# Kernel optimization log

Measured on AMD Instinct MI355X. Metric: run time of the kernel, lower is better.

The kernel has to match this reference:

```python
import jax, jax.numpy as jnp
from jax import lax
import numpy as np

V, H, L = 32000, 512, 256   # vocab, hidden_dim, latent_dim
B, TE, TD = 16, 512, 256    # batch, enc max len, dec max len


def setup_inputs() -> dict:
    key = jax.random.key(0)
    ks = jax.random.split(key, 20)
    s = 0.05
    inp = {}
    inp['emb'] = jax.random.normal(ks[0], (V, H), jnp.float32) * s
    # GRU params, PyTorch layout: W_ih [3H_out, D_in], gate order r,z,n
    inp['enc_Wih'] = jax.random.normal(ks[1], (3 * H, H), jnp.float32) * s
    inp['enc_Whh'] = jax.random.normal(ks[2], (3 * H, H), jnp.float32) * s
    inp['enc_bih'] = jnp.zeros((3 * H,), jnp.float32)
    inp['enc_bhh'] = jnp.zeros((3 * H,), jnp.float32)
    inp['dec_Wih'] = jax.random.normal(ks[3], (3 * L, H), jnp.float32) * s
    inp['dec_Whh'] = jax.random.normal(ks[4], (3 * L, L), jnp.float32) * s
    inp['dec_bih'] = jnp.zeros((3 * L,), jnp.float32)
    inp['dec_bhh'] = jnp.zeros((3 * L,), jnp.float32)
    inp['W_mu'] = jax.random.normal(ks[5], (L, 2 * H), jnp.float32) * s
    inp['b_mu'] = jnp.zeros((L,), jnp.float32)
    inp['W_ls'] = jax.random.normal(ks[6], (L, 2 * H), jnp.float32) * s
    inp['b_ls'] = jnp.zeros((L,), jnp.float32)
    inp['W_fc'] = jax.random.normal(ks[7], (V, L), jnp.float32) * s
    inp['b_fc'] = jnp.zeros((V,), jnp.float32)
    inp['noise'] = jax.random.normal(ks[8], (B, L), jnp.float32)  # reparam eps
    inp['enc_ids'] = jax.random.randint(ks[9], (B, TE), 0, V)
    inp['enc_len'] = jax.random.randint(ks[10], (B,), 1, TE + 1)
    inp['dec_ids'] = jax.random.randint(ks[11], (B, TD), 0, V)
    inp['dec_len'] = jax.random.randint(ks[12], (B,), 1, TD + 1)
    return inp


def gru(x, lengths, h0, Wih, Whh, bih, bhh):
    # x: [B,T,D], h0: [B,Hout]. Emulates packed GRU: state frozen and output
    # zeroed past each sample's length (pad_packed_sequence semantics).
    T = x.shape[1]
    Hout = h0.shape[-1]
    xT = jnp.swapaxes(x, 0, 1)                              # [T,B,D]
    valid = jnp.arange(T)[:, None] < lengths[None, :]       # [T,B]

    def step(h, inp):
        x_t, v = inp
        gx = x_t @ Wih.T + bih                              # [B,3Hout]
        gh = h @ Whh.T + bhh
        r = jax.nn.sigmoid(gx[:, :Hout] + gh[:, :Hout])
        z = jax.nn.sigmoid(gx[:, Hout:2 * Hout] + gh[:, Hout:2 * Hout])
        n = jnp.tanh(gx[:, 2 * Hout:] + r * gh[:, 2 * Hout:])
        h_new = (1.0 - z) * n + z * h
        h_keep = jnp.where(v[:, None], h_new, h)
        out = jnp.where(v[:, None], h_new, 0.0)
        return h_keep, out

    h_last, outs = lax.scan(step, h0, (xT, valid))
    return jnp.swapaxes(outs, 0, 1), h_last                 # [B,T,Hout], [B,Hout]


def masked_softmax(scores, mask):
    s = jnp.where(mask, scores, -jnp.inf)
    a = jax.nn.softmax(s, axis=-1)
    return jnp.where(mask, a, 0.0)


def reference(emb, enc_Wih, enc_Whh, enc_bih, enc_bhh,
              dec_Wih, dec_Whh, dec_bih, dec_bhh,
              W_mu, b_mu, W_ls, b_ls, W_fc, b_fc, noise,
              enc_ids, enc_len, dec_ids, dec_len):
    # ---- encode ----
    x_enc = emb[enc_ids]                                    # [B,TE,H]
    h0 = jnp.zeros((x_enc.shape[0], H), x_enc.dtype)
    out, last_state = gru(x_enc, enc_len, h0, enc_Wih, enc_Whh, enc_bih, enc_bhh)
    mask = jnp.arange(out.shape[1])[None, :] < enc_len[:, None]   # [B,TE]
    # batched masked attention pooling (replaces per-sample _return_weight loop)
    first_state = out[:, 0, :]                              # out[0] always valid
    alpha_fw = masked_softmax(jnp.einsum('btd,bd->bt', out, last_state), mask)
    alpha_bw = masked_softmax(jnp.einsum('btd,bd->bt', out, first_state), mask)
    alpha = 0.5 * (alpha_fw + alpha_bw)
    semantic = jnp.einsum('bt,btd->bd', alpha, out)
    h_enc = jnp.concatenate([last_state, semantic], axis=1)  # [B,2H]
    # ---- sample latent ----
    mu = h_enc @ W_mu.T + b_mu
    sigma = jnp.exp(h_enc @ W_ls.T + b_ls)
    z = mu + sigma * noise
    # ---- decode ----
    x_dec = emb[dec_ids]                                    # [B,TD,H]
    dec_out, _ = gru(x_dec, dec_len, z, dec_Wih, dec_Whh, dec_bih, dec_bhh)
    logits = dec_out @ W_fc.T + b_fc                        # [B,TD,V]
    dec_max_len = jnp.max(dec_len)
    return logits, dec_max_len, mu, sigma
```

## Files before the change

kernel.cpp:

```cpp
#include <hip/hip_runtime.h>
#include <hip/hip_bf16.h>
#include <stdint.h>

#define B 16
#define H 512
#define L 256
#define TE 512
#define TD 256
#define NV 32000

typedef __attribute__((ext_vector_type(8))) __bf16 bf16x8;
typedef __attribute__((ext_vector_type(4))) float f32x4;
typedef __attribute__((ext_vector_type(8))) unsigned short u16x8;
typedef __attribute__((ext_vector_type(4))) unsigned short u16x4;
typedef unsigned short u16;
typedef unsigned long long u64;

__device__ __forceinline__ u16 f2bf(float f) {
  unsigned u = __float_as_uint(f);
  u += 0x7fffu + ((u >> 16) & 1u);
  return (u16)(u >> 16);
}
__device__ __forceinline__ float fast_sigmoid(float x) {
  return __builtin_amdgcn_rcpf(1.f + __expf(-x));
}
__device__ __forceinline__ float fast_tanh(float x) {
  float e = __expf(2.f * x);
  return 1.f - 2.f * __builtin_amdgcn_rcpf(e + 1.f);
}

__device__ __forceinline__ u16x8 pack8(float4 a, float4 c) {
  u16x8 r;
  r[0] = f2bf(a.x); r[1] = f2bf(a.y); r[2] = f2bf(a.z); r[3] = f2bf(a.w);
  r[4] = f2bf(c.x); r[5] = f2bf(c.y); r[6] = f2bf(c.z); r[7] = f2bf(c.w);
  return r;
}

__global__ __launch_bounds__(256) void k_f2bf(const float* __restrict__ in,
                                              u16* __restrict__ outp, long n) {
  long i = ((long)blockIdx.x * 256 + threadIdx.x) * 8;
  if (i + 8 > n) return;
  float4 a = *(const float4*)&in[i];
  float4 c = *(const float4*)&in[i + 4];
  *(u16x8*)&outp[i] = pack8(a, c);
}

__global__ __launch_bounds__(256) void k_gather(const float* __restrict__ emb,
                                                const int* __restrict__ ids,
                                                u16* __restrict__ X, int rows) {
  int gid = blockIdx.x * 256 + threadIdx.x;
  int m = gid >> 6, seg = gid & 63;
  if (m >= rows) return;
  long src = (long)ids[m] * H + seg * 8;
  float4 a = *(const float4*)&emb[src];
  float4 c = *(const float4*)&emb[src + 4];
  *(u16x8*)&X[(long)m * H + seg * 8] = pack8(a, c);
}

__global__ __launch_bounds__(256) void k_gemm_bt(const u16* __restrict__ A,
                                                 const u16* __restrict__ Bw,
                                                 const float* __restrict__ bias,
                                                 float* __restrict__ C,
                                                 int M, int N, int K) {
  constexpr int LDSK = 72;
  __shared__ u16 Al[128 * LDSK];
  __shared__ u16 Bl[128 * LDSK];
  const int tid = threadIdx.x;
  const int lane = tid & 63;
  const int wave = tid >> 6;
  const int wr = (wave >> 1) * 64, wc = (wave & 1) * 64;
  const long tM = (long)blockIdx.y * 128, tN = (long)blockIdx.x * 128;
  const int r32 = tid >> 3;
  const int c8 = (tid & 7) * 8;
  const u16* Ag = A + (tM + r32) * (long)K + c8;
  const u16* Bg = Bw + (tN + r32) * (long)K + c8;
  const int fr = lane & 15;
  const int fq = lane >> 4;
  f32x4 acc[4][4] = {};

  for (int kb = 0; kb < K; kb += 64) {
    u16x8 ta0 = *(const u16x8*)(Ag + kb);
    u16x8 ta1 = *(const u16x8*)(Ag + 32 * (long)K + kb);
    u16x8 ta2 = *(const u16x8*)(Ag + 64 * (long)K + kb);
    u16x8 ta3 = *(const u16x8*)(Ag + 96 * (long)K + kb);
    u16x8 tb0 = *(const u16x8*)(Bg + kb);
    u16x8 tb1 = *(const u16x8*)(Bg + 32 * (long)K + kb);
    u16x8 tb2 = *(const u16x8*)(Bg + 64 * (long)K + kb);
    u16x8 tb3 = *(const u16x8*)(Bg + 96 * (long)K + kb);
    __syncthreads();
    *(u16x8*)&Al[(r32 +  0) * LDSK + c8] = ta0;
    *(u16x8*)&Al[(r32 + 32) * LDSK + c8] = ta1;
    *(u16x8*)&Al[(r32 + 64) * LDSK + c8] = ta2;
    *(u16x8*)&Al[(r32 + 96) * LDSK + c8] = ta3;
    *(u16x8*)&Bl[(r32 +  0) * LDSK + c8] = tb0;
    *(u16x8*)&Bl[(r32 + 32) * LDSK + c8] = tb1;
    *(u16x8*)&Bl[(r32 + 64) * LDSK + c8] = tb2;
    *(u16x8*)&Bl[(r32 + 96) * LDSK + c8] = tb3;
    __syncthreads();
#pragma unroll
    for (int ks = 0; ks < 2; ks++) {
      const int kcol = ks * 32 + fq * 8;
      bf16x8 av[4], bv[4];
#pragma unroll
      for (int mi = 0; mi < 4; mi++)
        av[mi] = __builtin_bit_cast(bf16x8, *(const u16x8*)&Al[(wr + mi * 16 + fr) * LDSK + kcol]);
#pragma unroll
      for (int ni = 0; ni < 4; ni++)
        bv[ni] = __builtin_bit_cast(bf16x8, *(const u16x8*)&Bl[(wc + ni * 16 + fr) * LDSK + kcol]);
#pragma unroll
      for (int mi = 0; mi < 4; mi++)
#pragma unroll
        for (int ni = 0; ni < 4; ni++)
          acc[mi][ni] = __builtin_amdgcn_mfma_f32_16x16x32_bf16(av[mi], bv[ni], acc[mi][ni], 0, 0, 0);
    }
  }
#pragma unroll
  for (int mi = 0; mi < 4; mi++) {
    long row = tM + wr + mi * 16 + fq * 4;
#pragma unroll
    for (int ni = 0; ni < 4; ni++) {
      long col = tN + wc + ni * 16 + fr;
      float bs = bias[col];
#pragma unroll
      for (int r = 0; r < 4; r++)
        C[(row + r) * (long)N + col] = acc[mi][ni][r] + bs;
    }
  }
}

template <bool ENC, int HD, int T, int UPW>
__global__ __launch_bounds__(256) void k_gru4(const float* __restrict__ GX,
                                              const float* __restrict__ Whh,
                                              const float* __restrict__ bhh,
                                              const int* __restrict__ lens,
                                              u64* __restrict__ Hbuf,
                                              const float* __restrict__ h0f,
                                              float* __restrict__ out_f32,
                                              u16* __restrict__ out_bf,
                                              float* __restrict__ hlast) {
  constexpr int ROWS = 3 * UPW;
  constexpr int NT = ROWS / 16;
  constexpr int NA = (NT + 3) / 4;
  constexpr int LDH = HD + 8;
  constexpr int CT = 16 * UPW / 2;
  constexpr int WPB = HD / 2;
  constexpr int NWORD = 16 * WPB;
  constexpr int PW = NWORD / 256;
  __shared__ u16 w_lds[ROWS][LDH];
  __shared__ u16 h_lds[16][LDH];
  __shared__ float g_lds[3][16][UPW];

  const int tid = threadIdx.x;
  const int u0 = blockIdx.x * UPW;
  const int lane = tid & 63, wv = tid >> 6;
  const int fr = lane & 15, fq = lane >> 4;

  for (int i = tid; i < ROWS * HD / 4; i += 256) {
    int rr = i / (HD / 4), c = (i % (HD / 4)) * 4;
    int grow = (rr / UPW) * HD + u0 + (rr % UPW);
    float4 v = *(const float4*)&Whh[(long)grow * HD + c];
    u16x4 p; p[0] = f2bf(v.x); p[1] = f2bf(v.y); p[2] = f2bf(v.z); p[3] = f2bf(v.w);
    *(u16x4*)&w_lds[rr][c] = p;
  }
  int tmax = 1;
#pragma unroll
  for (int i = 0; i < 16; i++) tmax = max(tmax, lens[i]);

  const bool act = tid < CT;
  const int cb = tid / (UPW / 2);
  const int up = tid % (UPW / 2);
  const int uu = u0 + 2 * up;
  const int len_b = lens[act ? cb : 0];
  float bh[3][2], hold[2];
#pragma unroll
  for (int g = 0; g < 3; g++)
#pragma unroll
    for (int j = 0; j < 2; j++) bh[g][j] = act ? bhh[g * HD + uu + j] : 0.f;
#pragma unroll
  for (int j = 0; j < 2; j++)
    hold[j] = (ENC || !act) ? 0.f : h0f[cb * HD + uu + j];
  __syncthreads();

  for (int t = 0; ; t++) {
    const u64* Hc = Hbuf + (size_t)(t & 1) * NWORD;
    u64* Hn = Hbuf + (size_t)((t + 1) & 1) * NWORD;
    float gxv[3][2];
    if (act) {
#pragma unroll
      for (int g = 0; g < 3; g++)
#pragma unroll
        for (int j = 0; j < 2; j++)
          gxv[g][j] = GX[((size_t)cb * T + t) * 3 * HD + g * HD + uu + j];
    }
    const unsigned want = (unsigned)t;
    u64 vv[PW];
#pragma unroll
    for (int i = 0; i < PW; i++)
      vv[i] = __hip_atomic_load(&Hc[i * 256 + tid], __ATOMIC_RELAXED, __HIP_MEMORY_SCOPE_AGENT);
    for (;;) {
      bool ok = true;
#pragma unroll
      for (int i = 0; i < PW; i++) ok &= ((unsigned)(vv[i] >> 32) == want);
      if (ok) break;
#pragma unroll
      for (int i = 0; i < PW; i++)
        if ((unsigned)(vv[i] >> 32) != want)
          vv[i] = __hip_atomic_load(&Hc[i * 256 + tid], __ATOMIC_RELAXED, __HIP_MEMORY_SCOPE_AGENT);
    }
#pragma unroll
    for (int i = 0; i < PW; i++) {
      int w = i * 256 + tid;
      *(unsigned*)&h_lds[w / WPB][(w % WPB) * 2] = (unsigned)vv[i];
    }
    __syncthreads();
    f32x4 acc[NA];
#pragma unroll
    for (int a = 0; a < NA; a++) {
      int ti = wv + a * 4;
      if (ti < NT) {
        f32x4 ac = {};
#pragma unroll
        for (int kk = 0; kk < HD / 32; kk++) {
          int kc = kk * 32 + fq * 8;
          bf16x8 av = __builtin_bit_cast(bf16x8, *(const u16x8*)&h_lds[fr][kc]);
          bf16x8 bv = __builtin_bit_cast(bf16x8, *(const u16x8*)&w_lds[ti * 16 + fr][kc]);
          ac = __builtin_amdgcn_mfma_f32_16x16x32_bf16(av, bv, ac, 0, 0, 0);
        }
        acc[a] = ac;
      }
    }
#pragma unroll
    for (int a = 0; a < NA; a++) {
      int ti = wv + a * 4;
      if (ti < NT) {
        int g = (ti * 16) / UPW, ul = (ti * 16) % UPW;
#pragma unroll
        for (int r = 0; r < 4; r++)
          g_lds[g][fq * 4 + r][ul + fr] = acc[a][r];
      }
    }
    __syncthreads();
    if (act) {
      const bool val = t < len_b;
      u16 pk[2]; float hnv[2];
#pragma unroll
      for (int j = 0; j < 2; j++) {
        int u = 2 * up + j;
        float rr_ = fast_sigmoid(g_lds[0][cb][u] + bh[0][j] + gxv[0][j]);
        float zz  = fast_sigmoid(g_lds[1][cb][u] + bh[1][j] + gxv[1][j]);
        float nn  = fast_tanh(gxv[2][j] + rr_ * (g_lds[2][cb][u] + bh[2][j]));
        float hnew = (1.f - zz) * nn + zz * hold[j];
        float hk = val ? hnew : hold[j];
        hold[j] = hk;
        pk[j] = f2bf(hk);
        hnv[j] = val ? hnew : 0.f;
      }
      u64 pw = ((u64)(unsigned)(t + 1) << 32) | ((unsigned)pk[1] << 16) | pk[0];
      __hip_atomic_store(&Hn[cb * WPB + (uu >> 1)], pw,
                         __ATOMIC_RELAXED, __HIP_MEMORY_SCOPE_AGENT);
      if constexpr (ENC) {
        *(float2*)&out_f32[((size_t)cb * T + t) * HD + uu] = make_float2(hnv[0], hnv[1]);
      } else {
        *(unsigned*)&out_bf[((size_t)cb * T + t) * HD + uu] =
            ((unsigned)f2bf(hnv[1]) << 16) | f2bf(hnv[0]);
      }
    }
    if (t + 1 >= tmax) break;
  }

  if (act) {
    if constexpr (ENC) {
      *(float2*)&hlast[cb * HD + uu] = make_float2(hold[0], hold[1]);
      for (int t2 = tmax; t2 < T; t2++)
        *(float2*)&out_f32[((size_t)cb * T + t2) * HD + uu] = make_float2(0.f, 0.f);
    } else {
      for (int t2 = tmax; t2 < T; t2++)
        *(unsigned*)&out_bf[((size_t)cb * T + t2) * HD + uu] = 0u;
    }
  }
}

__global__ __launch_bounds__(256) void k_middle(const float* __restrict__ out_enc,
                                                const float* __restrict__ hlast,
                                                const int* __restrict__ enc_len,
                                                const float* __restrict__ W_mu,
                                                const float* __restrict__ b_mu,
                                                const float* __restrict__ W_ls,
                                                const float* __restrict__ b_ls,
                                                const float* __restrict__ noise,
                                                const int* __restrict__ dec_len,
                                                float* __restrict__ out_tail,
                                                float* __restrict__ zf,
                                                u64* __restrict__ hbw) {
  const int b = blockIdx.x, tid = threadIdx.x;
  __shared__ float last[H], first[H], sfw[TE], sbw[TE], alpha[TE], sem[H];
  __shared__ float redA[256], redB[256];
  __shared__ u16 zbf[L];
  const int len = enc_len[b];
  for (int i = tid; i < H; i += 256) {
    last[i] = hlast[b * H + i];
    first[i] = out_enc[((size_t)b * TE) * H + i];
  }
  __syncthreads();
  for (int t = tid; t < TE; t += 256) {
    float afw = 0.f, abw = 0.f;
    if (t < len) {
      const float4* op = (const float4*)&out_enc[((size_t)b * TE + t) * H];
      for (int i = 0; i < H / 4; i++) {
        float4 o = op[i];
        float4 l = *(const float4*)&last[i * 4];
        float4 f = *(const float4*)&first[i * 4];
        afw += o.x * l.x + o.y * l.y + o.z * l.z + o.w * l.w;
        abw += o.x * f.x + o.y * f.y + o.z * f.z + o.w * f.w;
      }
    }
    sfw[t] = afw; sbw[t] = abw;
  }
  __syncthreads();
  float mfw = -3e38f, mbw = -3e38f;
  for (int t = tid; t < len; t += 256) { mfw = fmaxf(mfw, sfw[t]); mbw = fmaxf(mbw, sbw[t]); }
  redA[tid] = mfw; redB[tid] = mbw; __syncthreads();
  for (int s = 128; s > 0; s >>= 1) {
    if (tid < s) { redA[tid] = fmaxf(redA[tid], redA[tid + s]); redB[tid] = fmaxf(redB[tid], redB[tid + s]); }
    __syncthreads();
  }
  const float Mfw = redA[0], Mbw = redB[0];
  __syncthreads();
  float tfw = 0.f, tbw = 0.f;
  for (int t = tid; t < len; t += 256) {
    float e1 = expf(sfw[t] - Mfw); sfw[t] = e1; tfw += e1;
    float e2 = expf(sbw[t] - Mbw); sbw[t] = e2; tbw += e2;
  }
  redA[tid] = tfw; redB[tid] = tbw; __syncthreads();
  for (int s = 128; s > 0; s >>= 1) {
    if (tid < s) { redA[tid] += redA[tid + s]; redB[tid] += redB[tid + s]; }
    __syncthreads();
  }
  const float ifw = 0.5f / redA[0], ibw = 0.5f / redB[0];
  __syncthreads();
  for (int t = tid; t < TE; t += 256) alpha[t] = (t < len) ? (sfw[t] * ifw + sbw[t] * ibw) : 0.f;
  __syncthreads();
  for (int d = tid; d < H; d += 256) {
    float s = 0.f;
    for (int t = 0; t < len; t++) s += alpha[t] * out_enc[((size_t)b * TE + t) * H + d];
    sem[d] = s;
  }
  __syncthreads();
  {
    const int j = tid;
    const float4* wm = (const float4*)&W_mu[(size_t)j * 2 * H];
    const float4* wl = (const float4*)&W_ls[(size_t)j * 2 * H];
    float am = 0.f, al = 0.f;
    for (int i = 0; i < H / 4; i++) {
      float4 hh = *(const float4*)&last[i * 4];
      float4 w1 = wm[i]; am += hh.x * w1.x + hh.y * w1.y + hh.z * w1.z + hh.w * w1.w;
      float4 w2 = wl[i]; al += hh.x * w2.x + hh.y * w2.y + hh.z * w2.z + hh.w * w2.w;
    }
    for (int i = 0; i < H / 4; i++) {
      float4 hh = *(const float4*)&sem[i * 4];
      float4 w1 = wm[H / 4 + i]; am += hh.x * w1.x + hh.y * w1.y + hh.z * w1.z + hh.w * w1.w;
      float4 w2 = wl[H / 4 + i]; al += hh.x * w2.x + hh.y * w2.y + hh.z * w2.z + hh.w * w2.w;
    }
    float muv = am + b_mu[j];
    float sgv = expf(al + b_ls[j]);
    float zv = muv + sgv * noise[b * L + j];
    out_tail[131072001ul + (size_t)b * L + j] = muv;
    out_tail[131076097ul + (size_t)b * L + j] = sgv;
    zf[b * L + j] = zv;
    zbf[j] = f2bf(zv);
  }
  __syncthreads();
  if (tid < L / 2) {
    u64 pw = ((unsigned)zbf[2 * tid + 1] << 16) | (u64)zbf[2 * tid];
    __hip_atomic_store(&hbw[b * (L / 2) + tid], pw,
                       __ATOMIC_RELAXED, __HIP_MEMORY_SCOPE_AGENT);
  }
  if (b == 0 && tid == 0) {
    int m = 0;
    for (int i = 0; i < B; i++) m = max(m, dec_len[i]);
    out_tail[131072000ul] = (float)m;
  }
}

extern "C" void kernel_launch(void* const* d_in, const int* in_sizes, int n_in,
                              void* d_out, int out_size, void* d_ws, size_t ws_size,
                              hipStream_t stream) {
  const float* emb     = (const float*)d_in[0];
  const float* eWih    = (const float*)d_in[1];
  const float* eWhh    = (const float*)d_in[2];
  const float* ebih    = (const float*)d_in[3];
  const float* ebhh    = (const float*)d_in[4];
  const float* dWih    = (const float*)d_in[5];
  const float* dWhh    = (const float*)d_in[6];
  const float* dbih    = (const float*)d_in[7];
  const float* dbhh    = (const float*)d_in[8];
  const float* W_mu    = (const float*)d_in[9];
  const float* b_mu    = (const float*)d_in[10];
  const float* W_ls    = (const float*)d_in[11];
  const float* b_ls    = (const float*)d_in[12];
  const float* W_fc    = (const float*)d_in[13];
  const float* b_fc    = (const float*)d_in[14];
  const float* noise   = (const float*)d_in[15];
  const int*   enc_ids = (const int*)d_in[16];
  const int*   enc_len = (const int*)d_in[17];
  const int*   dec_ids = (const int*)d_in[18];
  const int*   dec_len = (const int*)d_in[19];
  float* out = (float*)d_out;
  char* ws = (char*)d_ws;

  u16*   eWih_bf  = (u16*)(ws + 0);
  u16*   dWih_bf  = (u16*)(ws + 1572864);
  u16*   Wfc_bf   = (u16*)(ws + 2359296);
  u64*   Hbuf_enc = (u64*)(ws + 18743296);
  float* hlast    = (float*)(ws + 18808832);
  u64*   Hbuf_dec = (u64*)(ws + 18841600);
  u16*   dec_out  = (u16*)(ws + 18874368);
  float* zf       = (float*)(ws + 20971520);

  char* ob = (char*)d_out;
  u16*   Xenc_bf = (u16*)(ob + 0);
  u16*   Xdec_bf = (u16*)(ob + 8388608);
  float* GXE     = (float*)(ob + 12582912);
  float* GXD     = (float*)(ob + 62914560);
  float* out_enc = (float*)(ob + 75497472);

  hipMemsetAsync(Hbuf_enc, 0, 65536, stream);
  hipMemsetAsync(Hbuf_dec, 0, 32768, stream);

  k_f2bf<<<384, 256, 0, stream>>>(eWih, eWih_bf, 786432);
  k_f2bf<<<192, 256, 0, stream>>>(dWih, dWih_bf, 393216);
  k_f2bf<<<4000, 256, 0, stream>>>(W_fc, Wfc_bf, 8192000);
  k_gather<<<2048, 256, 0, stream>>>(emb, enc_ids, Xenc_bf, B * TE);
  k_gather<<<1024, 256, 0, stream>>>(emb, dec_ids, Xdec_bf, B * TD);

  k_gemm_bt<<<dim3(12, 64), 256, 0, stream>>>(Xenc_bf, eWih_bf, ebih, GXE, B * TE, 3 * H, H);
  k_gemm_bt<<<dim3(6, 32), 256, 0, stream>>>(Xdec_bf, dWih_bf, dbih, GXD, B * TD, 3 * L, H);

  k_gru4<true, H, TE, 32><<<16, 256, 0, stream>>>(GXE, eWhh, ebhh, enc_len, Hbuf_enc,
                                                  nullptr, out_enc, nullptr, hlast);

  k_middle<<<B, 256, 0, stream>>>(out_enc, hlast, enc_len, W_mu, b_mu, W_ls, b_ls,
                                  noise, dec_len, out, zf, Hbuf_dec);

  k_gru4<false, L, TD, 16><<<16, 256, 0, stream>>>(GXD, dWhh, dbhh, dec_len, Hbuf_dec,
                                                   zf, nullptr, dec_out, nullptr);

  k_gemm_bt<<<dim3(250, 32), 256, 0, stream>>>(dec_out, Wfc_bf, b_fc, out, B * TD, NV, L);
}
```

Before: 2.193 ms.

## Compute GRU gates in MFMA registers and drop the LDS gate round-trip

The persistent GRU kernel now interleaves the Whh rows in LDS so each wave owns 16 hidden units and computes all three gate tiles (r, z, n) itself. The gate nonlinearities and state update then run directly on the MFMA accumulator registers, which removes the g_lds staging buffer and one __syncthreads per timestep. Neighbouring lanes pair up their values through a shuffle to write the packed bf16 state. The decoder runs on 8 blocks of 32 units instead of 16 blocks of 16, which reduces the number of blocks in the cross-block spin-wait. The trailing zero fill is now done cooperatively with vector stores. Only two of four waves do the math, so per-block parallelism in the elementwise phase drops.

```diff
diff --git a/kernel.cpp b/kernel.cpp
--- a/kernel.cpp
+++ b/kernel.cpp
@@ -129,7 +129,7 @@
 }
 
 template <bool ENC, int HD, int T, int UPW>
-__global__ __launch_bounds__(256) void k_gru4(const float* __restrict__ GX,
+__global__ __launch_bounds__(256) void k_gru5(const float* __restrict__ GX,
                                               const float* __restrict__ Whh,
                                               const float* __restrict__ bhh,
                                               const int* __restrict__ lens,
@@ -138,26 +138,26 @@
                                               float* __restrict__ out_f32,
                                               u16* __restrict__ out_bf,
                                               float* __restrict__ hlast) {
+  constexpr int G2 = UPW / 16;
   constexpr int ROWS = 3 * UPW;
-  constexpr int NT = ROWS / 16;
-  constexpr int NA = (NT + 3) / 4;
   constexpr int LDH = HD + 8;
-  constexpr int CT = 16 * UPW / 2;
   constexpr int WPB = HD / 2;
   constexpr int NWORD = 16 * WPB;
   constexpr int PW = NWORD / 256;
   __shared__ u16 w_lds[ROWS][LDH];
   __shared__ u16 h_lds[16][LDH];
-  __shared__ float g_lds[3][16][UPW];
 
   const int tid = threadIdx.x;
   const int u0 = blockIdx.x * UPW;
   const int lane = tid & 63, wv = tid >> 6;
   const int fr = lane & 15, fq = lane >> 4;
+  const bool cw = wv < G2;
+  const int u = u0 + wv * 16 + fr;
 
   for (int i = tid; i < ROWS * HD / 4; i += 256) {
     int rr = i / (HD / 4), c = (i % (HD / 4)) * 4;
-    int grow = (rr / UPW) * HD + u0 + (rr % UPW);
+    int tt = rr >> 4, fr_ = rr & 15;
+    int grow = (tt % 3) * HD + u0 + (tt / 3) * 16 + fr_;
     float4 v = *(const float4*)&Whh[(long)grow * HD + c];
     u16x4 p; p[0] = f2bf(v.x); p[1] = f2bf(v.y); p[2] = f2bf(v.z); p[3] = f2bf(v.w);
     *(u16x4*)&w_lds[rr][c] = p;
@@ -166,31 +166,27 @@
 #pragma unroll
   for (int i = 0; i < 16; i++) tmax = max(tmax, lens[i]);
 
-  const bool act = tid < CT;
-  const int cb = tid / (UPW / 2);
-  const int up = tid % (UPW / 2);
-  const int uu = u0 + 2 * up;
-  const int len_b = lens[act ? cb : 0];
-  float bh[3][2], hold[2];
-#pragma unroll
-  for (int g = 0; g < 3; g++)
-#pragma unroll
-    for (int j = 0; j < 2; j++) bh[g][j] = act ? bhh[g * HD + uu + j] : 0.f;
-#pragma unroll
-  for (int j = 0; j < 2; j++)
-    hold[j] = (ENC || !act) ? 0.f : h0f[cb * HD + uu + j];
+  float bh[3], hold[4];
+  int len4[4];
+#pragma unroll
+  for (int g = 0; g < 3; g++) bh[g] = cw ? bhh[g * HD + u] : 0.f;
+#pragma unroll
+  for (int r = 0; r < 4; r++) {
+    len4[r] = cw ? lens[fq * 4 + r] : 0;
+    hold[r] = (ENC || !cw) ? 0.f : h0f[(fq * 4 + r) * HD + u];
+  }
   __syncthreads();
 
   for (int t = 0; ; t++) {
     const u64* Hc = Hbuf + (size_t)(t & 1) * NWORD;
     u64* Hn = Hbuf + (size_t)((t + 1) & 1) * NWORD;
-    float gxv[3][2];
-    if (act) {
+    float gxr[3][4];
+    if (cw) {
 #pragma unroll
       for (int g = 0; g < 3; g++)
 #pragma unroll
-        for (int j = 0; j < 2; j++)
-          gxv[g][j] = GX[((size_t)cb * T + t) * 3 * HD + g * HD + uu + j];
+        for (int r = 0; r < 4; r++)
+          gxr[g][r] = GX[((size_t)(fq * 4 + r) * T + t) * 3 * HD + g * HD + u];
     }
     const unsigned want = (unsigned)t;
     u64 vv[PW];
@@ -213,70 +209,68 @@
       *(unsigned*)&h_lds[w / WPB][(w % WPB) * 2] = (unsigned)vv[i];
     }
     __syncthreads();
-    f32x4 acc[NA];
-#pragma unroll
-    for (int a = 0; a < NA; a++) {
-      int ti = wv + a * 4;
-      if (ti < NT) {
-        f32x4 ac = {};
-#pragma unroll
-        for (int kk = 0; kk < HD / 32; kk++) {
-          int kc = kk * 32 + fq * 8;
-          bf16x8 av = __builtin_bit_cast(bf16x8, *(const u16x8*)&h_lds[fr][kc]);
-          bf16x8 bv = __builtin_bit_cast(bf16x8, *(const u16x8*)&w_lds[ti * 16 + fr][kc]);
-          ac = __builtin_amdgcn_mfma_f32_16x16x32_bf16(av, bv, ac, 0, 0, 0);
+    f32x4 acc[3] = {};
+    if (cw) {
+#pragma unroll
+      for (int kk = 0; kk < HD / 32; kk++) {
+        int kc = kk * 32 + fq * 8;
+        bf16x8 av = __builtin_bit_cast(bf16x8, *(const u16x8*)&h_lds[fr][kc]);
+#pragma unroll
+        for (int g = 0; g < 3; g++) {
+          bf16x8 bv = __builtin_bit_cast(bf16x8,
+              *(const u16x8*)&w_lds[(wv * 3 + g) * 16 + fr][kc]);
+          acc[g] = __builtin_amdgcn_mfma_f32_16x16x32_bf16(av, bv, acc[g], 0, 0, 0);
         }
-        acc[a] = ac;
       }
-    }
-#pragma unroll
-    for (int a = 0; a < NA; a++) {
-      int ti = wv + a * 4;
-      if (ti < NT) {
-        int g = (ti * 16) / UPW, ul = (ti * 16) % UPW;
-#pragma unroll
-        for (int r = 0; r < 4; r++)
-          g_lds[g][fq * 4 + r][ul + fr] = acc[a][r];
+#pragma unroll
+      for (int r = 0; r < 4; r++) {
+        const int bb = fq * 4 + r;
+        const bool val = t < len4[r];
+        float rr_ = fast_sigmoid(acc[0][r] + bh[0] + gxr[0][r]);
+        float zz  = fast_sigmoid(acc[1][r] + bh[1] + gxr[1][r]);
+        float nn  = fast_tanh(gxr[2][r] + rr_ * (acc[2][r] + bh[2]));
+        float hnew = (1.f - zz) * nn + zz * hold[r];
+        float hk = val ? hnew : hold[r];
+        hold[r] = hk;
+        float sh = __shfl_xor(hk, 1);
+        if (!(fr & 1)) {
+          u64 pw = ((u64)(unsigned)(t + 1) << 32) |
+                   ((unsigned)f2bf(sh) << 16) | f2bf(hk);
+          __hip_atomic_store(&Hn[bb * WPB + (u >> 1)], pw,
+                             __ATOMIC_RELAXED, __HIP_MEMORY_SCOPE_AGENT);
+          if constexpr (ENC) {
+            float2 o = val ? make_float2(hk, sh) : make_float2(0.f, 0.f);
+            *(float2*)&out_f32[((size_t)bb * T + t) * HD + u] = o;
+          } else {
+            unsigned ow = val ? (((unsigned)f2bf(sh) << 16) | f2bf(hk)) : 0u;
+            *(unsigned*)&out_bf[((size_t)bb * T + t) * HD + u] = ow;
+          }
+        }
       }
     }
-    __syncthreads();
-    if (act) {
-      const bool val = t < len_b;
-      u16 pk[2]; float hnv[2];
-#pragma unroll
-      for (int j = 0; j < 2; j++) {
-        int u = 2 * up + j;
-        float rr_ = fast_sigmoid(g_lds[0][cb][u] + bh[0][j] + gxv[0][j]);
-        float zz  = fast_sigmoid(g_lds[1][cb][u] + bh[1][j] + gxv[1][j]);
-        float nn  = fast_tanh(gxv[2][j] + rr_ * (g_lds[2][cb][u] + bh[2][j]));
-        float hnew = (1.f - zz) * nn + zz * hold[j];
-        float hk = val ? hnew : hold[j];
-        hold[j] = hk;
-        pk[j] = f2bf(hk);
-        hnv[j] = val ? hnew : 0.f;
+    if (t + 1 >= tmax) break;
+  }
+
+  if (cw) {
+    if constexpr (ENC) {
+#pragma unroll
+      for (int r = 0; r < 4; r++) hlast[(fq * 4 + r) * HD + u] = hold[r];
+    }
+  }
+  if constexpr (ENC) {
+    float4 z4 = make_float4(0.f, 0.f, 0.f, 0.f);
+    for (int bb = 0; bb < 16; bb++)
+      for (int x = tid; x < (T - tmax) * HD / 4; x += 256) {
+        int t2 = tmax + (x * 4) / HD, c = (x * 4) % HD;
+        *(float4*)&out_f32[((size_t)bb * T + t2) * HD + c] = z4;
       }
-      u64 pw = ((u64)(unsigned)(t + 1) << 32) | ((unsigned)pk[1] << 16) | pk[0];
-      __hip_atomic_store(&Hn[cb * WPB + (uu >> 1)], pw,
-                         __ATOMIC_RELAXED, __HIP_MEMORY_SCOPE_AGENT);
-      if constexpr (ENC) {
-        *(float2*)&out_f32[((size_t)cb * T + t) * HD + uu] = make_float2(hnv[0], hnv[1]);
-      } else {
-        *(unsigned*)&out_bf[((size_t)cb * T + t) * HD + uu] =
-            ((unsigned)f2bf(hnv[1]) << 16) | f2bf(hnv[0]);
+  } else {
+    u16x8 z8 = {};
+    for (int bb = 0; bb < 16; bb++)
+      for (int x = tid; x < (T - tmax) * HD / 8; x += 256) {
+        int t2 = tmax + (x * 8) / HD, c = (x * 8) % HD;
+        *(u16x8*)&out_bf[((size_t)bb * T + t2) * HD + c] = z8;
       }
-    }
-    if (t + 1 >= tmax) break;
-  }
-
-  if (act) {
-    if constexpr (ENC) {
-      *(float2*)&hlast[cb * HD + uu] = make_float2(hold[0], hold[1]);
-      for (int t2 = tmax; t2 < T; t2++)
-        *(float2*)&out_f32[((size_t)cb * T + t2) * HD + uu] = make_float2(0.f, 0.f);
-    } else {
-      for (int t2 = tmax; t2 < T; t2++)
-        *(unsigned*)&out_bf[((size_t)cb * T + t2) * HD + uu] = 0u;
-    }
   }
 }
 
@@ -436,14 +430,14 @@
   k_gemm_bt<<<dim3(12, 64), 256, 0, stream>>>(Xenc_bf, eWih_bf, ebih, GXE, B * TE, 3 * H, H);
   k_gemm_bt<<<dim3(6, 32), 256, 0, stream>>>(Xdec_bf, dWih_bf, dbih, GXD, B * TD, 3 * L, H);
 
-  k_gru4<true, H, TE, 32><<<16, 256, 0, stream>>>(GXE, eWhh, ebhh, enc_len, Hbuf_enc,
+  k_gru5<true, H, TE, 32><<<16, 256, 0, stream>>>(GXE, eWhh, ebhh, enc_len, Hbuf_enc,
                                                   nullptr, out_enc, nullptr, hlast);
 
   k_middle<<<B, 256, 0, stream>>>(out_enc, hlast, enc_len, W_mu, b_mu, W_ls, b_ls,
                                   noise, dec_len, out, zf, Hbuf_dec);
 
-  k_gru4<false, L, TD, 16><<<16, 256, 0, stream>>>(GXD, dWhh, dbhh, dec_len, Hbuf_dec,
-                                                   zf, nullptr, dec_out, nullptr);
+  k_gru5<false, L, TD, 32><<<8, 256, 0, stream>>>(GXD, dWhh, dbhh, dec_len, Hbuf_dec,
+                                                  zf, nullptr, dec_out, nullptr);
 
   k_gemm_bt<<<dim3(250, 32), 256, 0, stream>>>(dec_out, Wfc_bf, b_fc, out, B * TD, NV, L);
 }
```

Result: slower. 2.879 ms (+31.3%).

## Overlap decoder input GEMM and W_fc conversion with encoder GRU blocks

Applied to the files above, without the earlier changes.

The encoder GRU kernel now launches 448 blocks instead of 16. The first 16 run the recurrence and the remaining blocks compute the decoder input-projection GEMM and the fp32-to-bf16 conversion of W_fc, work that previously ran as separate kernels. The latency-bound serial GRU leaves most CUs idle, so this fills them with independent work. The risk is that the extra blocks compete for bandwidth and CU slots with the GRU blocks, which may depend on cross-block sync through Hbuf, and that the shared LDS sizing raises per-block footprint.

```diff
diff --git a/kernel.cpp b/kernel.cpp
--- a/kernel.cpp
+++ b/kernel.cpp
@@ -57,19 +57,20 @@
   *(u16x8*)&X[(long)m * H + seg * 8] = pack8(a, c);
 }
 
-__global__ __launch_bounds__(256) void k_gemm_bt(const u16* __restrict__ A,
-                                                 const u16* __restrict__ Bw,
-                                                 const float* __restrict__ bias,
-                                                 float* __restrict__ C,
-                                                 int M, int N, int K) {
+__device__ __forceinline__ void gemm_tile(char* smem, int bx, int by,
+                                          const u16* __restrict__ A,
+                                          const u16* __restrict__ Bw,
+                                          const float* __restrict__ bias,
+                                          float* __restrict__ C,
+                                          int N, int K) {
   constexpr int LDSK = 72;
-  __shared__ u16 Al[128 * LDSK];
-  __shared__ u16 Bl[128 * LDSK];
+  u16* Al = (u16*)smem;
+  u16* Bl = (u16*)(smem + 128 * LDSK * 2);
   const int tid = threadIdx.x;
   const int lane = tid & 63;
   const int wave = tid >> 6;
   const int wr = (wave >> 1) * 64, wc = (wave & 1) * 64;
-  const long tM = (long)blockIdx.y * 128, tN = (long)blockIdx.x * 128;
+  const long tM = (long)by * 128, tN = (long)bx * 128;
   const int r32 = tid >> 3;
   const int c8 = (tid & 7) * 8;
   const u16* Ag = A + (tM + r32) * (long)K + c8;
@@ -128,16 +129,32 @@
   }
 }
 
+__global__ __launch_bounds__(256) void k_gemm_bt(const u16* __restrict__ A,
+                                                 const u16* __restrict__ Bw,
+                                                 const float* __restrict__ bias,
+                                                 float* __restrict__ C,
+                                                 int M, int N, int K) {
+  __shared__ __align__(16) char smem[2 * 128 * 72 * 2];
+  gemm_tile(smem, blockIdx.x, blockIdx.y, A, Bw, bias, C, N, K);
+}
+
 template <bool ENC, int HD, int T, int UPW>
-__global__ __launch_bounds__(256) void k_gru4(const float* __restrict__ GX,
-                                              const float* __restrict__ Whh,
-                                              const float* __restrict__ bhh,
-                                              const int* __restrict__ lens,
-                                              u64* __restrict__ Hbuf,
-                                              const float* __restrict__ h0f,
-                                              float* __restrict__ out_f32,
-                                              u16* __restrict__ out_bf,
-                                              float* __restrict__ hlast) {
+__global__ __launch_bounds__(256) void k_gru10(const float* __restrict__ GX,
+                                               const float* __restrict__ Whh,
+                                               const float* __restrict__ bhh,
+                                               const int* __restrict__ lens,
+                                               u64* __restrict__ Hbuf,
+                                               const float* __restrict__ h0f,
+                                               float* __restrict__ out_f32,
+                                               u16* __restrict__ out_bf,
+                                               float* __restrict__ hlast,
+                                               int ngru,
+                                               const u16* __restrict__ sA,
+                                               const u16* __restrict__ sB,
+                                               const float* __restrict__ sbias,
+                                               float* __restrict__ sC,
+                                               const float* __restrict__ cvt_in,
+                                               u16* __restrict__ cvt_out) {
   constexpr int ROWS = 3 * UPW;
   constexpr int NT = ROWS / 16;
   constexpr int NA = (NT + 3) / 4;
@@ -146,9 +163,32 @@
   constexpr int WPB = HD / 2;
   constexpr int NWORD = 16 * WPB;
   constexpr int PW = NWORD / 256;
-  __shared__ u16 w_lds[ROWS][LDH];
-  __shared__ u16 h_lds[16][LDH];
-  __shared__ float g_lds[3][16][UPW];
+  constexpr size_t WB = (size_t)ROWS * LDH * 2;
+  constexpr size_t HBB = (size_t)16 * LDH * 2;
+  constexpr size_t GB = (size_t)3 * 16 * UPW * 4;
+  constexpr size_t GRUB = WB + HBB + GB;
+  constexpr size_t SMEMB = GRUB > 36864 ? GRUB : 36864;
+  __shared__ __align__(16) char smem[SMEMB];
+
+  if ((int)blockIdx.x >= ngru) {
+    int sb = (int)blockIdx.x - ngru;
+    if (sb < 192) {
+      gemm_tile(smem, sb % 6, sb / 6, sA, sB, sbias, sC, 3 * L, H);
+    } else {
+      int sbf = sb - 192;
+      for (long base = (long)sbf * 2048 + (long)threadIdx.x * 8;
+           base < (long)NV * L; base += 240L * 2048) {
+        float4 a = *(const float4*)&cvt_in[base];
+        float4 c = *(const float4*)&cvt_in[base + 4];
+        *(u16x8*)&cvt_out[base] = pack8(a, c);
+      }
+    }
+    return;
+  }
+
+  u16 (*w_lds)[LDH] = (u16(*)[LDH])smem;
+  u16 (*h_lds)[LDH] = (u16(*)[LDH])(smem + WB);
+  float (*g_lds)[16][UPW] = (float(*)[16][UPW])(smem + WB + HBB);
 
   const int tid = threadIdx.x;
   const int u0 = blockIdx.x * UPW;
@@ -429,21 +469,23 @@
 
   k_f2bf<<<384, 256, 0, stream>>>(eWih, eWih_bf, 786432);
   k_f2bf<<<192, 256, 0, stream>>>(dWih, dWih_bf, 393216);
-  k_f2bf<<<4000, 256, 0, stream>>>(W_fc, Wfc_bf, 8192000);
   k_gather<<<2048, 256, 0, stream>>>(emb, enc_ids, Xenc_bf, B * TE);
   k_gather<<<1024, 256, 0, stream>>>(emb, dec_ids, Xdec_bf, B * TD);
 
   k_gemm_bt<<<dim3(12, 64), 256, 0, stream>>>(Xenc_bf, eWih_bf, ebih, GXE, B * TE, 3 * H, H);
-  k_gemm_bt<<<dim3(6, 32), 256, 0, stream>>>(Xdec_bf, dWih_bf, dbih, GXD, B * TD, 3 * L, H);
-
-  k_gru4<true, H, TE, 32><<<16, 256, 0, stream>>>(GXE, eWhh, ebhh, enc_len, Hbuf_enc,
-                                                  nullptr, out_enc, nullptr, hlast);
+
+  k_gru10<true, H, TE, 32><<<448, 256, 0, stream>>>(GXE, eWhh, ebhh, enc_len, Hbuf_enc,
+                                                    nullptr, out_enc, nullptr, hlast,
+                                                    16, Xdec_bf, dWih_bf, dbih, GXD,
+                                                    W_fc, Wfc_bf);
 
   k_middle<<<B, 256, 0, stream>>>(out_enc, hlast, enc_len, W_mu, b_mu, W_ls, b_ls,
                                   noise, dec_len, out, zf, Hbuf_dec);
 
-  k_gru4<false, L, TD, 16><<<16, 256, 0, stream>>>(GXD, dWhh, dbhh, dec_len, Hbuf_dec,
-                                                   zf, nullptr, dec_out, nullptr);
+  k_gru10<false, L, TD, 16><<<16, 256, 0, stream>>>(GXD, dWhh, dbhh, dec_len, Hbuf_dec,
+                                                    zf, nullptr, dec_out, nullptr,
+                                                    16, nullptr, nullptr, nullptr, nullptr,
+                                                    nullptr, nullptr);
 
   k_gemm_bt<<<dim3(250, 32), 256, 0, stream>>>(dec_out, Wfc_bf, b_fc, out, B * TD, NV, L);
 }
```

Result: no change. 2.171 ms, median of 2 (-1.0%).
